# Performance work log

Hardware: AMD Instinct MI355X
Metric: run time of the kernel (lower is better)

The kernel has to match this reference:

```python
import jax, jax.numpy as jnp
import numpy as np

N_NODES = 50000
N_EDGES = 800000


def _gcn_conv(x, W, b, src, dst, deg_inv_sqrt, n_nodes):
    # PyG GCNConv: h = x @ W, then symmetric-normalized sum aggregation
    h = x @ W  # [N, F_out]
    norm = deg_inv_sqrt[src] * deg_inv_sqrt[dst]  # [E_aug]
    msg = h[src] * norm[:, None]  # [E_aug, F_out]
    out = jax.ops.segment_sum(msg, dst, num_segments=n_nodes)
    return out + b


def setup_inputs() -> dict:
    key = jax.random.key(0)
    k1, k2, k3, k4 = jax.random.split(key, 4)
    x = jax.random.normal(k1, (N_NODES, 128), dtype=jnp.float32)
    edge_index = jax.random.randint(k2, (2, N_EDGES), 0, N_NODES, dtype=jnp.int64)
    W1 = jax.random.normal(k3, (128, 64), dtype=jnp.float32) * (1.0 / np.sqrt(128))
    b1 = jnp.zeros((64,), dtype=jnp.float32)
    W2 = jax.random.normal(k4, (64, 32), dtype=jnp.float32) * (1.0 / np.sqrt(64))
    b2 = jnp.zeros((32,), dtype=jnp.float32)
    return {"x": x, "edge_index": edge_index, "W1": W1, "b1": b1, "W2": W2, "b2": b2}


def reference(x, edge_index, W1, b1, W2, b2):
    n_nodes = x.shape[0]
    # add self-loops (PyG GCNConv default)
    loop = jnp.arange(n_nodes, dtype=edge_index.dtype)
    src = jnp.concatenate([edge_index[0], loop])
    dst = jnp.concatenate([edge_index[1], loop])
    # symmetric normalization: deg from target index (gcn_norm)
    deg = jax.ops.segment_sum(jnp.ones_like(dst, dtype=x.dtype), dst, num_segments=n_nodes)
    deg_inv_sqrt = jnp.where(deg > 0, jax.lax.rsqrt(jnp.maximum(deg, 1.0)), 0.0)

    h = _gcn_conv(x, W1, b1, src, dst, deg_inv_sqrt, n_nodes)
    h = jax.nn.relu(h)
    # dropout is identity in eval mode (reference runs inference)
    out = _gcn_conv(h, W2, b2, src, dst, deg_inv_sqrt, n_nodes)
    return out
```

## Files before the change

### kernel.cpp

```cpp
#include <hip/hip_runtime.h>
#include <hip/hip_fp16.h>


#define F_IN 128
#define F_MID 64
#define F_OUT 32
#define NBLK 256

#define RFL(x) __builtin_amdgcn_readfirstlane(x)

__device__ __forceinline__ void h8acc(float* a, const uint4& v) {
    const __half2* hp = (const __half2*)&v;
#pragma unroll
    for (int i = 0; i < 4; ++i) {
        float2 f = __half22float2(hp[i]);
        a[2 * i]     += f.x;
        a[2 * i + 1] += f.y;
    }
}

__device__ __forceinline__ uint4 pack8(const float4& a, const float4& b) {
    union { uint4 u; __half2 h[4]; } pk;
    pk.h[0] = __float22half2_rn(make_float2(a.x, a.y));
    pk.h[1] = __float22half2_rn(make_float2(a.z, a.w));
    pk.h[2] = __float22half2_rn(make_float2(b.x, b.y));
    pk.h[3] = __float22half2_rn(make_float2(b.z, b.w));
    return pk.u;
}

__global__ __launch_bounds__(256) void k_hist(
    const int* __restrict__ dst, int E, int chunk, int nbuk,
    int* __restrict__ blockHist) {
    __shared__ int cnt[256];
    int t = threadIdx.x;
    cnt[t] = 0;
    __syncthreads();
    int e0 = blockIdx.x * chunk;
    int e1 = min(E, e0 + chunk);
    for (int e = e0 + t; e < e1; e += 256)
        atomicAdd(&cnt[dst[e] >> 8], 1);
    __syncthreads();
    if (t < nbuk) blockHist[blockIdx.x * nbuk + t] = cnt[t];
}

__global__ __launch_bounds__(NBLK) void k_scan_buckets(
    const int* __restrict__ blockHist, int nbuk,
    int* __restrict__ blockOff, int* __restrict__ bucketTotal) {
    __shared__ int s[NBLK];
    int b = blockIdx.x;
    int t = threadIdx.x;
    int v = blockHist[t * nbuk + b];
    s[t] = v;
    __syncthreads();
    for (int o = 1; o < NBLK; o <<= 1) {
        int add = (t >= o) ? s[t - o] : 0;
        __syncthreads();
        s[t] += add;
        __syncthreads();
    }
    blockOff[t * nbuk + b] = s[t] - v;
    if (t == NBLK - 1) bucketTotal[b] = s[t];
}

__global__ __launch_bounds__(256) void k_scan_starts(
    const int* __restrict__ bucketTotal, int nbuk, int E,
    int* __restrict__ bucketStart) {
    __shared__ int s[256];
    int t = threadIdx.x;
    int v = (t < nbuk) ? bucketTotal[t] : 0;
    s[t] = v;
    __syncthreads();
    for (int o = 1; o < 256; o <<= 1) {
        int add = (t >= o) ? s[t - o] : 0;
        __syncthreads();
        s[t] += add;
        __syncthreads();
    }
    if (t < nbuk) bucketStart[t] = s[t] - v;
    if (t == 0) bucketStart[nbuk] = E;
}

__global__ __launch_bounds__(256) void k_scatter_edges(
    const int* __restrict__ src, const int* __restrict__ dst, int E, int chunk,
    int nbuk, const int* __restrict__ blockOff, const int* __restrict__ bucketStart,
    int* __restrict__ esort) {
    __shared__ int off[256];
    int t = threadIdx.x;
    if (t < nbuk) off[t] = blockOff[blockIdx.x * nbuk + t] + bucketStart[t];
    __syncthreads();
    int e0 = blockIdx.x * chunk;
    int e1 = min(E, e0 + chunk);
    for (int e = e0 + t; e < e1; e += 256) {
        int d = dst[e];
        int pos = atomicAdd(&off[d >> 8], 1);
        esort[pos] = (src[e] << 8) | (d & 255);
    }
}

__global__ __launch_bounds__(256) void k_bucket_csr(
    const int* __restrict__ esort, const int* __restrict__ bucketStart, int n,
    int* __restrict__ rowstart, int* __restrict__ deg, float* __restrict__ dis,
    int* __restrict__ col) {
    __shared__ int cnt[256];
    __shared__ int s[256];
    __shared__ int cur[256];
    int b = blockIdx.x;
    int t = threadIdx.x;
    int node0 = b << 8;
    int e0 = bucketStart[b], e1 = bucketStart[b + 1];
    cnt[t] = 0;
    __syncthreads();
    for (int e = e0 + t; e < e1; e += 256)
        atomicAdd(&cnt[esort[e] & 255], 1);
    __syncthreads();
    int v = cnt[t];
    s[t] = v;
    __syncthreads();
    for (int o = 1; o < 256; o <<= 1) {
        int add = (t >= o) ? s[t - o] : 0;
        __syncthreads();
        s[t] += add;
        __syncthreads();
    }
    int ex = s[t] - v;
    cur[t] = ex;
    int node = node0 + t;
    if (node < n) {
        rowstart[node] = e0 + ex;
        deg[node] = v;
        dis[node] = rsqrtf((float)(v + 1));
    }
    __syncthreads();
    for (int e = e0 + t; e < e1; e += 256) {
        int p = esort[e];
        int pos = atomicAdd(&cur[p & 255], 1);
        col[e0 + pos] = p >> 8;
    }
}

__global__ __launch_bounds__(256, 4) void k_gemm1(
    const float* __restrict__ x, const float* __restrict__ W1,
    const float* __restrict__ dis, uint4* __restrict__ g1h, int n) {
    __shared__ float xs[64 * 129];
    int tid  = threadIdx.x;
    int row0 = blockIdx.x * 64;
    for (int i = tid; i < 64 * F_IN; i += 256) {
        int r = i >> 7, k = i & 127;
        int gr = row0 + r;
        xs[r * 129 + k] = (gr < n) ? x[(size_t)gr * F_IN + k] : 0.0f;
    }
    __syncthreads();
    int w = RFL(tid >> 6);
    int r = tid & 63;
    const float4* W4 = (const float4*)W1;
    float4 a0 = {0.f,0.f,0.f,0.f}, a1 = a0, a2 = a0, a3 = a0;
#pragma unroll 4
    for (int k = 0; k < F_IN; ++k) {
        float xv = xs[r * 129 + k];
        float4 w0 = W4[k * 16 + w * 4 + 0];
        float4 w1 = W4[k * 16 + w * 4 + 1];
        float4 w2 = W4[k * 16 + w * 4 + 2];
        float4 w3 = W4[k * 16 + w * 4 + 3];
        a0.x += xv * w0.x; a0.y += xv * w0.y; a0.z += xv * w0.z; a0.w += xv * w0.w;
        a1.x += xv * w1.x; a1.y += xv * w1.y; a1.z += xv * w1.z; a1.w += xv * w1.w;
        a2.x += xv * w2.x; a2.y += xv * w2.y; a2.z += xv * w2.z; a2.w += xv * w2.w;
        a3.x += xv * w3.x; a3.y += xv * w3.y; a3.z += xv * w3.z; a3.w += xv * w3.w;
    }
    int gr = row0 + r;
    if (gr < n) {
        float dv = dis[gr];
        a0.x *= dv; a0.y *= dv; a0.z *= dv; a0.w *= dv;
        a1.x *= dv; a1.y *= dv; a1.z *= dv; a1.w *= dv;
        a2.x *= dv; a2.y *= dv; a2.z *= dv; a2.w *= dv;
        a3.x *= dv; a3.y *= dv; a3.z *= dv; a3.w *= dv;
        g1h[(size_t)gr * 8 + w * 2 + 0] = pack8(a0, a1);
        g1h[(size_t)gr * 8 + w * 2 + 1] = pack8(a2, a3);
    }
}

__global__ __launch_bounds__(256) void k_gather1(
    const int* __restrict__ rowstart, const int* __restrict__ deg,
    const int* __restrict__ col, const uint4* __restrict__ g1h,
    const float* __restrict__ dis, const float* __restrict__ b1,
    float* __restrict__ h, int n) {
    int wave = RFL(threadIdx.x >> 6);
    int lane = threadIdx.x & 63;
    int q    = lane & 7;
    int slot = lane >> 3;
    int d    = blockIdx.x * 4 + wave;
    if (d >= n) return;
    int base = RFL(rowstart[d]);
    int cnt  = RFL(deg[d]);
    float a[8] = {0,0,0,0,0,0,0,0};
    float b[8] = {0,0,0,0,0,0,0,0};
    if (slot == 0) {
        uint4 v = g1h[(size_t)d * 8 + q];
        h8acc(a, v);
    }
    int j = 0;
    for (; j + 16 <= cnt; j += 16) {
        int s0 = col[base + j + slot];
        int s1 = col[base + j + 8 + slot];
        uint4 v0 = g1h[(size_t)s0 * 8 + q];
        uint4 v1 = g1h[(size_t)s1 * 8 + q];
        h8acc(a, v0);
        h8acc(b, v1);
    }
    for (; j + 8 <= cnt; j += 8) {
        int s = col[base + j + slot];
        uint4 v = g1h[(size_t)s * 8 + q];
        h8acc(a, v);
    }
    if (slot < cnt - j) {
        int s = col[base + j + slot];
        uint4 v = g1h[(size_t)s * 8 + q];
        h8acc(a, v);
    }
#pragma unroll
    for (int i = 0; i < 8; ++i) a[i] += b[i];
#pragma unroll
    for (int i = 0; i < 8; ++i) a[i] += __shfl_xor(a[i], 8);
#pragma unroll
    for (int i = 0; i < 8; ++i) a[i] += __shfl_xor(a[i], 16);
#pragma unroll
    for (int i = 0; i < 8; ++i) a[i] += __shfl_xor(a[i], 32);
    if (slot == 0) {
        float dv = dis[d];
        float4 bv0 = ((const float4*)b1)[q * 2 + 0];
        float4 bv1 = ((const float4*)b1)[q * 2 + 1];
        float4 o0, o1;
        o0.x = fmaxf(a[0] * dv + bv0.x, 0.f);
        o0.y = fmaxf(a[1] * dv + bv0.y, 0.f);
        o0.z = fmaxf(a[2] * dv + bv0.z, 0.f);
        o0.w = fmaxf(a[3] * dv + bv0.w, 0.f);
        o1.x = fmaxf(a[4] * dv + bv1.x, 0.f);
        o1.y = fmaxf(a[5] * dv + bv1.y, 0.f);
        o1.z = fmaxf(a[6] * dv + bv1.z, 0.f);
        o1.w = fmaxf(a[7] * dv + bv1.w, 0.f);
        float4* H4 = (float4*)h;
        H4[(size_t)d * 16 + q * 2 + 0] = o0;
        H4[(size_t)d * 16 + q * 2 + 1] = o1;
    }
}

__global__ __launch_bounds__(256, 4) void k_gemm2(
    const float* __restrict__ h, const float* __restrict__ W2,
    const float* __restrict__ dis, uint4* __restrict__ g2h, int n) {
    __shared__ float hs[64 * 65];
    int tid  = threadIdx.x;
    int row0 = blockIdx.x * 64;
    for (int i = tid; i < 64 * F_MID; i += 256) {
        int r = i >> 6, k = i & 63;
        int gr = row0 + r;
        hs[r * 65 + k] = (gr < n) ? h[(size_t)gr * F_MID + k] : 0.0f;
    }
    __syncthreads();
    int w = RFL(tid >> 6);
    int r = tid & 63;
    const float4* W4 = (const float4*)W2;
    float4 a0 = {0.f,0.f,0.f,0.f}, a1 = a0;
#pragma unroll 4
    for (int k = 0; k < F_MID; ++k) {
        float hv = hs[r * 65 + k];
        float4 w0 = W4[k * 8 + w * 2 + 0];
        float4 w1 = W4[k * 8 + w * 2 + 1];
        a0.x += hv * w0.x; a0.y += hv * w0.y; a0.z += hv * w0.z; a0.w += hv * w0.w;
        a1.x += hv * w1.x; a1.y += hv * w1.y; a1.z += hv * w1.z; a1.w += hv * w1.w;
    }
    int gr = row0 + r;
    if (gr < n) {
        float dv = dis[gr];
        a0.x *= dv; a0.y *= dv; a0.z *= dv; a0.w *= dv;
        a1.x *= dv; a1.y *= dv; a1.z *= dv; a1.w *= dv;
        g2h[(size_t)gr * 4 + w] = pack8(a0, a1);
    }
}

__global__ __launch_bounds__(256) void k_gather2(
    const int* __restrict__ rowstart, const int* __restrict__ deg,
    const int* __restrict__ col, const uint4* __restrict__ g2h,
    const float* __restrict__ dis, const float* __restrict__ b2,
    float* __restrict__ out, int n) {
    int wave = RFL(threadIdx.x >> 6);
    int lane = threadIdx.x & 63;
    int q    = lane & 3;
    int slot = lane >> 2;
    int d    = blockIdx.x * 4 + wave;
    if (d >= n) return;
    int base = RFL(rowstart[d]);
    int cnt  = RFL(deg[d]);
    float a[8] = {0,0,0,0,0,0,0,0};
    float b[8] = {0,0,0,0,0,0,0,0};
    if (slot == 0) {
        uint4 v = g2h[(size_t)d * 4 + q];
        h8acc(a, v);
    }
    int j = 0;
    for (; j + 32 <= cnt; j += 32) {
        int s0 = col[base + j + slot];
        int s1 = col[base + j + 16 + slot];
        uint4 v0 = g2h[(size_t)s0 * 4 + q];
        uint4 v1 = g2h[(size_t)s1 * 4 + q];
        h8acc(a, v0);
        h8acc(b, v1);
    }
    for (; j + 16 <= cnt; j += 16) {
        int s = col[base + j + slot];
        uint4 v = g2h[(size_t)s * 4 + q];
        h8acc(a, v);
    }
    if (slot < cnt - j) {
        int s = col[base + j + slot];
        uint4 v = g2h[(size_t)s * 4 + q];
        h8acc(a, v);
    }
#pragma unroll
    for (int i = 0; i < 8; ++i) a[i] += b[i];
#pragma unroll
    for (int i = 0; i < 8; ++i) a[i] += __shfl_xor(a[i], 4);
#pragma unroll
    for (int i = 0; i < 8; ++i) a[i] += __shfl_xor(a[i], 8);
#pragma unroll
    for (int i = 0; i < 8; ++i) a[i] += __shfl_xor(a[i], 16);
#pragma unroll
    for (int i = 0; i < 8; ++i) a[i] += __shfl_xor(a[i], 32);
    if (slot == 0) {
        float dv = dis[d];
        float4 bv0 = ((const float4*)b2)[q * 2 + 0];
        float4 bv1 = ((const float4*)b2)[q * 2 + 1];
        float4 o0, o1;
        o0.x = a[0] * dv + bv0.x;
        o0.y = a[1] * dv + bv0.y;
        o0.z = a[2] * dv + bv0.z;
        o0.w = a[3] * dv + bv0.w;
        o1.x = a[4] * dv + bv1.x;
        o1.y = a[5] * dv + bv1.y;
        o1.z = a[6] * dv + bv1.z;
        o1.w = a[7] * dv + bv1.w;
        float4* O4 = (float4*)out;
        O4[(size_t)d * 8 + q * 2 + 0] = o0;
        O4[(size_t)d * 8 + q * 2 + 1] = o1;
    }
}

extern "C" void kernel_launch(void* const* d_in, const int* in_sizes, int n_in,
                              void* d_out, int out_size, void* d_ws, size_t ws_size,
                              hipStream_t stream) {
    const float* x  = (const float*)d_in[0];
    const int*   ei = (const int*)d_in[1];
    const float* W1 = (const float*)d_in[2];
    const float* b1 = (const float*)d_in[3];
    const float* W2 = (const float*)d_in[4];
    const float* b2 = (const float*)d_in[5];

    int n = in_sizes[0] / F_IN;
    int E = in_sizes[1] / 2;
    const int* src = ei;
    const int* dst = ei + E;

    int nbuk  = (n + 255) >> 8;
    int chunk = (E + NBLK - 1) / NBLK;

    char* ws = (char*)d_ws;
    size_t off = 0;
    auto alloc = [&](size_t bytes) {
        char* p = ws + off;
        off += (bytes + 255) & ~(size_t)255;
        return p;
    };
    int*   blockHist   = (int*)  alloc((size_t)NBLK * nbuk * 4);
    int*   blockOff    = (int*)  alloc((size_t)NBLK * nbuk * 4);
    int*   bucketTotal = (int*)  alloc((size_t)nbuk * 4);
    int*   bucketStart = (int*)  alloc((size_t)(nbuk + 1) * 4);
    int*   esort       = (int*)  alloc((size_t)E * 4);
    int*   col         = (int*)  alloc((size_t)E * 4);
    int*   rowstart    = (int*)  alloc((size_t)n * 4);
    int*   deg         = (int*)  alloc((size_t)n * 4);
    float* dis         = (float*)alloc((size_t)n * 4);
    uint4* g1h         = (uint4*)alloc((size_t)n * F_MID * 2);
    float* h           = (float*)alloc((size_t)n * F_MID * 4);
    uint4* g2h         = (uint4*)alloc((size_t)n * F_OUT * 2);

    k_hist<<<NBLK, 256, 0, stream>>>(dst, E, chunk, nbuk, blockHist);
    k_scan_buckets<<<nbuk, NBLK, 0, stream>>>(blockHist, nbuk, blockOff, bucketTotal);
    k_scan_starts<<<1, 256, 0, stream>>>(bucketTotal, nbuk, E, bucketStart);
    k_scatter_edges<<<NBLK, 256, 0, stream>>>(src, dst, E, chunk, nbuk, blockOff,
                                              bucketStart, esort);
    k_bucket_csr<<<nbuk, 256, 0, stream>>>(esort, bucketStart, n, rowstart, deg, dis, col);

    k_gemm1<<<(n + 63) / 64, 256, 0, stream>>>(x, W1, dis, g1h, n);
    k_gather1<<<(n + 3) / 4, 256, 0, stream>>>(rowstart, deg, col, g1h, dis, b1, h, n);
    k_gemm2<<<(n + 63) / 64, 256, 0, stream>>>(h, W2, dis, g2h, n);
    k_gather2<<<(n + 3) / 4, 256, 0, stream>>>(rowstart, deg, col, g2h, dis, b2,
                                               (float*)d_out, n);
}
```

Measured before the change: 184.7 us.

## Replace per-node CSR gather with bucket-level LDS atomic scatter aggregation

Drops the second sorting pass that built a full CSR (rowstart, deg, col) and keeps only the coarse 256-node bucket sort. Each block now owns one bucket of 256 destination nodes, seeds a shared-memory accumulator with the self-loop features, and scatters neighbor features into it with LDS float atomics before applying norm, bias and ReLU. This removes the CSR construction kernel's scan and col writes and the per-node load imbalance. In exchange it adds heavy LDS atomic traffic, a large shared-memory footprint that limits occupancy (about 66KB for layer 1), and only 196 blocks per gather, so there may be too little parallelism to hide latency. Floating-point summation order also becomes nondeterministic.

```diff
diff --git a/kernel.cpp b/kernel.cpp
--- a/kernel.cpp
+++ b/kernel.cpp
@@ -9,13 +9,13 @@
 
 #define RFL(x) __builtin_amdgcn_readfirstlane(x)
 
-__device__ __forceinline__ void h8acc(float* a, const uint4& v) {
+__device__ __forceinline__ void h8unpack(float* f, const uint4& v) {
     const __half2* hp = (const __half2*)&v;
 #pragma unroll
     for (int i = 0; i < 4; ++i) {
-        float2 f = __half22float2(hp[i]);
-        a[2 * i]     += f.x;
-        a[2 * i + 1] += f.y;
+        float2 t = __half22float2(hp[i]);
+        f[2 * i]     = t.x;
+        f[2 * i + 1] = t.y;
     }
 }
 
@@ -97,45 +97,20 @@
     }
 }
 
-__global__ __launch_bounds__(256) void k_bucket_csr(
+__global__ __launch_bounds__(256) void k_deg_dis(
     const int* __restrict__ esort, const int* __restrict__ bucketStart, int n,
-    int* __restrict__ rowstart, int* __restrict__ deg, float* __restrict__ dis,
-    int* __restrict__ col) {
+    float* __restrict__ dis) {
     __shared__ int cnt[256];
-    __shared__ int s[256];
-    __shared__ int cur[256];
     int b = blockIdx.x;
     int t = threadIdx.x;
-    int node0 = b << 8;
+    cnt[t] = 0;
+    __syncthreads();
     int e0 = bucketStart[b], e1 = bucketStart[b + 1];
-    cnt[t] = 0;
-    __syncthreads();
     for (int e = e0 + t; e < e1; e += 256)
         atomicAdd(&cnt[esort[e] & 255], 1);
     __syncthreads();
-    int v = cnt[t];
-    s[t] = v;
-    __syncthreads();
-    for (int o = 1; o < 256; o <<= 1) {
-        int add = (t >= o) ? s[t - o] : 0;
-        __syncthreads();
-        s[t] += add;
-        __syncthreads();
-    }
-    int ex = s[t] - v;
-    cur[t] = ex;
-    int node = node0 + t;
-    if (node < n) {
-        rowstart[node] = e0 + ex;
-        deg[node] = v;
-        dis[node] = rsqrtf((float)(v + 1));
-    }
-    __syncthreads();
-    for (int e = e0 + t; e < e1; e += 256) {
-        int p = esort[e];
-        int pos = atomicAdd(&cur[p & 255], 1);
-        col[e0 + pos] = p >> 8;
-    }
+    int node = (b << 8) + t;
+    if (node < n) dis[node] = rsqrtf((float)(cnt[t] + 1));
 }
 
 __global__ __launch_bounds__(256, 4) void k_gemm1(
@@ -178,68 +153,82 @@
     }
 }
 
-__global__ __launch_bounds__(256) void k_gather1(
-    const int* __restrict__ rowstart, const int* __restrict__ deg,
-    const int* __restrict__ col, const uint4* __restrict__ g1h,
-    const float* __restrict__ dis, const float* __restrict__ b1,
-    float* __restrict__ h, int n) {
-    int wave = RFL(threadIdx.x >> 6);
-    int lane = threadIdx.x & 63;
-    int q    = lane & 7;
-    int slot = lane >> 3;
-    int d    = blockIdx.x * 4 + wave;
-    if (d >= n) return;
-    int base = RFL(rowstart[d]);
-    int cnt  = RFL(deg[d]);
-    float a[8] = {0,0,0,0,0,0,0,0};
-    float b[8] = {0,0,0,0,0,0,0,0};
-    if (slot == 0) {
-        uint4 v = g1h[(size_t)d * 8 + q];
-        h8acc(a, v);
-    }
-    int j = 0;
-    for (; j + 16 <= cnt; j += 16) {
-        int s0 = col[base + j + slot];
-        int s1 = col[base + j + 8 + slot];
-        uint4 v0 = g1h[(size_t)s0 * 8 + q];
-        uint4 v1 = g1h[(size_t)s1 * 8 + q];
-        h8acc(a, v0);
-        h8acc(b, v1);
-    }
-    for (; j + 8 <= cnt; j += 8) {
-        int s = col[base + j + slot];
-        uint4 v = g1h[(size_t)s * 8 + q];
-        h8acc(a, v);
-    }
-    if (slot < cnt - j) {
-        int s = col[base + j + slot];
-        uint4 v = g1h[(size_t)s * 8 + q];
-        h8acc(a, v);
-    }
-#pragma unroll
-    for (int i = 0; i < 8; ++i) a[i] += b[i];
-#pragma unroll
-    for (int i = 0; i < 8; ++i) a[i] += __shfl_xor(a[i], 8);
-#pragma unroll
-    for (int i = 0; i < 8; ++i) a[i] += __shfl_xor(a[i], 16);
-#pragma unroll
-    for (int i = 0; i < 8; ++i) a[i] += __shfl_xor(a[i], 32);
-    if (slot == 0) {
-        float dv = dis[d];
-        float4 bv0 = ((const float4*)b1)[q * 2 + 0];
-        float4 bv1 = ((const float4*)b1)[q * 2 + 1];
-        float4 o0, o1;
-        o0.x = fmaxf(a[0] * dv + bv0.x, 0.f);
-        o0.y = fmaxf(a[1] * dv + bv0.y, 0.f);
-        o0.z = fmaxf(a[2] * dv + bv0.z, 0.f);
-        o0.w = fmaxf(a[3] * dv + bv0.w, 0.f);
-        o1.x = fmaxf(a[4] * dv + bv1.x, 0.f);
-        o1.y = fmaxf(a[5] * dv + bv1.y, 0.f);
-        o1.z = fmaxf(a[6] * dv + bv1.z, 0.f);
-        o1.w = fmaxf(a[7] * dv + bv1.w, 0.f);
-        float4* H4 = (float4*)h;
-        H4[(size_t)d * 16 + q * 2 + 0] = o0;
-        H4[(size_t)d * 16 + q * 2 + 1] = o1;
+__global__ __launch_bounds__(256) void k_bgather1(
+    const int* __restrict__ esort, const int* __restrict__ bucketStart,
+    const uint4* __restrict__ g1h, const float* __restrict__ dis,
+    const float* __restrict__ b1, float4* __restrict__ h4, int n) {
+    __shared__ float acc[256 * 65];
+    int b = blockIdx.x;
+    int t = threadIdx.x;
+    int node0 = b << 8;
+    for (int i = t; i < 256 * 8; i += 256) {
+        int dloc = i >> 3, q = i & 7;
+        int node = node0 + dloc;
+        float f[8] = {0,0,0,0,0,0,0,0};
+        if (node < n) {
+            uint4 v = g1h[(size_t)node * 8 + q];
+            h8unpack(f, v);
+        }
+        float* base = &acc[dloc * 65 + q * 8];
+#pragma unroll
+        for (int k = 0; k < 8; ++k) base[k] = f[k];
+    }
+    __syncthreads();
+    int e0 = bucketStart[b], e1 = bucketStart[b + 1];
+    int wave = RFL(t >> 6);
+    int lane = t & 63;
+    int slot = lane & 7;
+    int q    = lane >> 3;
+    int e = e0 + wave * 16;
+    for (; e + 16 <= e1; e += 64) {
+        int pA = esort[e + slot];
+        int pB = esort[e + 8 + slot];
+        uint4 vA = g1h[(size_t)(pA >> 8) * 8 + q];
+        uint4 vB = g1h[(size_t)(pB >> 8) * 8 + q];
+        float fA[8], fB[8];
+        h8unpack(fA, vA);
+        h8unpack(fB, vB);
+        float* bA = &acc[(pA & 255) * 65 + q * 8];
+        float* bB = &acc[(pB & 255) * 65 + q * 8];
+#pragma unroll
+        for (int k = 0; k < 8; ++k) atomicAdd(&bA[k], fA[k]);
+#pragma unroll
+        for (int k = 0; k < 8; ++k) atomicAdd(&bB[k], fB[k]);
+    }
+    int rem = e1 - e;
+    if (slot < rem) {
+        int p = esort[e + slot];
+        uint4 v = g1h[(size_t)(p >> 8) * 8 + q];
+        float f[8];
+        h8unpack(f, v);
+        float* ba = &acc[(p & 255) * 65 + q * 8];
+#pragma unroll
+        for (int k = 0; k < 8; ++k) atomicAdd(&ba[k], f[k]);
+    }
+    if (8 + slot < rem) {
+        int p = esort[e + 8 + slot];
+        uint4 v = g1h[(size_t)(p >> 8) * 8 + q];
+        float f[8];
+        h8unpack(f, v);
+        float* ba = &acc[(p & 255) * 65 + q * 8];
+#pragma unroll
+        for (int k = 0; k < 8; ++k) atomicAdd(&ba[k], f[k]);
+    }
+    __syncthreads();
+    const float4* B4 = (const float4*)b1;
+    for (int i = t; i < 256 * 16; i += 256) {
+        int dloc = i >> 4, c = i & 15;
+        int node = node0 + dloc;
+        if (node >= n) continue;
+        float dv = dis[node];
+        float* ap = &acc[dloc * 65 + c * 4];
+        float4 bv = B4[c];
+        float4 o;
+        o.x = fmaxf(ap[0] * dv + bv.x, 0.f);
+        o.y = fmaxf(ap[1] * dv + bv.y, 0.f);
+        o.z = fmaxf(ap[2] * dv + bv.z, 0.f);
+        o.w = fmaxf(ap[3] * dv + bv.w, 0.f);
+        h4[(size_t)node * 16 + c] = o;
     }
 }
 
@@ -276,70 +265,82 @@
     }
 }
 
-__global__ __launch_bounds__(256) void k_gather2(
-    const int* __restrict__ rowstart, const int* __restrict__ deg,
-    const int* __restrict__ col, const uint4* __restrict__ g2h,
-    const float* __restrict__ dis, const float* __restrict__ b2,
-    float* __restrict__ out, int n) {
-    int wave = RFL(threadIdx.x >> 6);
-    int lane = threadIdx.x & 63;
-    int q    = lane & 3;
-    int slot = lane >> 2;
-    int d    = blockIdx.x * 4 + wave;
-    if (d >= n) return;
-    int base = RFL(rowstart[d]);
-    int cnt  = RFL(deg[d]);
-    float a[8] = {0,0,0,0,0,0,0,0};
-    float b[8] = {0,0,0,0,0,0,0,0};
-    if (slot == 0) {
-        uint4 v = g2h[(size_t)d * 4 + q];
-        h8acc(a, v);
-    }
-    int j = 0;
-    for (; j + 32 <= cnt; j += 32) {
-        int s0 = col[base + j + slot];
-        int s1 = col[base + j + 16 + slot];
-        uint4 v0 = g2h[(size_t)s0 * 4 + q];
-        uint4 v1 = g2h[(size_t)s1 * 4 + q];
-        h8acc(a, v0);
-        h8acc(b, v1);
-    }
-    for (; j + 16 <= cnt; j += 16) {
-        int s = col[base + j + slot];
-        uint4 v = g2h[(size_t)s * 4 + q];
-        h8acc(a, v);
-    }
-    if (slot < cnt - j) {
-        int s = col[base + j + slot];
-        uint4 v = g2h[(size_t)s * 4 + q];
-        h8acc(a, v);
-    }
-#pragma unroll
-    for (int i = 0; i < 8; ++i) a[i] += b[i];
-#pragma unroll
-    for (int i = 0; i < 8; ++i) a[i] += __shfl_xor(a[i], 4);
-#pragma unroll
-    for (int i = 0; i < 8; ++i) a[i] += __shfl_xor(a[i], 8);
-#pragma unroll
-    for (int i = 0; i < 8; ++i) a[i] += __shfl_xor(a[i], 16);
-#pragma unroll
-    for (int i = 0; i < 8; ++i) a[i] += __shfl_xor(a[i], 32);
-    if (slot == 0) {
-        float dv = dis[d];
-        float4 bv0 = ((const float4*)b2)[q * 2 + 0];
-        float4 bv1 = ((const float4*)b2)[q * 2 + 1];
-        float4 o0, o1;
-        o0.x = a[0] * dv + bv0.x;
-        o0.y = a[1] * dv + bv0.y;
-        o0.z = a[2] * dv + bv0.z;
-        o0.w = a[3] * dv + bv0.w;
-        o1.x = a[4] * dv + bv1.x;
-        o1.y = a[5] * dv + bv1.y;
-        o1.z = a[6] * dv + bv1.z;
-        o1.w = a[7] * dv + bv1.w;
-        float4* O4 = (float4*)out;
-        O4[(size_t)d * 8 + q * 2 + 0] = o0;
-        O4[(size_t)d * 8 + q * 2 + 1] = o1;
+__global__ __launch_bounds__(256) void k_bgather2(
+    const int* __restrict__ esort, const int* __restrict__ bucketStart,
+    const uint4* __restrict__ g2h, const float* __restrict__ dis,
+    const float* __restrict__ b2, float4* __restrict__ out4, int n) {
+    __shared__ float acc[256 * 33];
+    int b = blockIdx.x;
+    int t = threadIdx.x;
+    int node0 = b << 8;
+    for (int i = t; i < 256 * 4; i += 256) {
+        int dloc = i >> 2, q = i & 3;
+        int node = node0 + dloc;
+        float f[8] = {0,0,0,0,0,0,0,0};
+        if (node < n) {
+            uint4 v = g2h[(size_t)node * 4 + q];
+            h8unpack(f, v);
+        }
+        float* base = &acc[dloc * 33 + q * 8];
+#pragma unroll
+        for (int k = 0; k < 8; ++k) base[k] = f[k];
+    }
+    __syncthreads();
+    int e0 = bucketStart[b], e1 = bucketStart[b + 1];
+    int wave = RFL(t >> 6);
+    int lane = t & 63;
+    int slot = lane & 15;
+    int q    = lane >> 4;
+    int e = e0 + wave * 32;
+    for (; e + 32 <= e1; e += 128) {
+        int pA = esort[e + slot];
+        int pB = esort[e + 16 + slot];
+        uint4 vA = g2h[(size_t)(pA >> 8) * 4 + q];
+        uint4 vB = g2h[(size_t)(pB >> 8) * 4 + q];
+        float fA[8], fB[8];
+        h8unpack(fA, vA);
+        h8unpack(fB, vB);
+        float* bA = &acc[(pA & 255) * 33 + q * 8];
+        float* bB = &acc[(pB & 255) * 33 + q * 8];
+#pragma unroll
+        for (int k = 0; k < 8; ++k) atomicAdd(&bA[k], fA[k]);
+#pragma unroll
+        for (int k = 0; k < 8; ++k) atomicAdd(&bB[k], fB[k]);
+    }
+    int rem = e1 - e;
+    if (slot < rem) {
+        int p = esort[e + slot];
+        uint4 v = g2h[(size_t)(p >> 8) * 4 + q];
+        float f[8];
+        h8unpack(f, v);
+        float* ba = &acc[(p & 255) * 33 + q * 8];
+#pragma unroll
+        for (int k = 0; k < 8; ++k) atomicAdd(&ba[k], f[k]);
+    }
+    if (16 + slot < rem) {
+        int p = esort[e + 16 + slot];
+        uint4 v = g2h[(size_t)(p >> 8) * 4 + q];
+        float f[8];
+        h8unpack(f, v);
+        float* ba = &acc[(p & 255) * 33 + q * 8];
+#pragma unroll
+        for (int k = 0; k < 8; ++k) atomicAdd(&ba[k], f[k]);
+    }
+    __syncthreads();
+    const float4* B4 = (const float4*)b2;
+    for (int i = t; i < 256 * 8; i += 256) {
+        int dloc = i >> 3, c = i & 7;
+        int node = node0 + dloc;
+        if (node >= n) continue;
+        float dv = dis[node];
+        float* ap = &acc[dloc * 33 + c * 4];
+        float4 bv = B4[c];
+        float4 o;
+        o.x = ap[0] * dv + bv.x;
+        o.y = ap[1] * dv + bv.y;
+        o.z = ap[2] * dv + bv.z;
+        o.w = ap[3] * dv + bv.w;
+        out4[(size_t)node * 8 + c] = o;
     }
 }
 
@@ -373,9 +374,6 @@
     int*   bucketTotal = (int*)  alloc((size_t)nbuk * 4);
     int*   bucketStart = (int*)  alloc((size_t)(nbuk + 1) * 4);
     int*   esort       = (int*)  alloc((size_t)E * 4);
-    int*   col         = (int*)  alloc((size_t)E * 4);
-    int*   rowstart    = (int*)  alloc((size_t)n * 4);
-    int*   deg         = (int*)  alloc((size_t)n * 4);
     float* dis         = (float*)alloc((size_t)n * 4);
     uint4* g1h         = (uint4*)alloc((size_t)n * F_MID * 2);
     float* h           = (float*)alloc((size_t)n * F_MID * 4);
@@ -386,11 +384,12 @@
     k_scan_starts<<<1, 256, 0, stream>>>(bucketTotal, nbuk, E, bucketStart);
     k_scatter_edges<<<NBLK, 256, 0, stream>>>(src, dst, E, chunk, nbuk, blockOff,
                                               bucketStart, esort);
-    k_bucket_csr<<<nbuk, 256, 0, stream>>>(esort, bucketStart, n, rowstart, deg, dis, col);
+    k_deg_dis<<<nbuk, 256, 0, stream>>>(esort, bucketStart, n, dis);
 
     k_gemm1<<<(n + 63) / 64, 256, 0, stream>>>(x, W1, dis, g1h, n);
-    k_gather1<<<(n + 3) / 4, 256, 0, stream>>>(rowstart, deg, col, g1h, dis, b1, h, n);
+    k_bgather1<<<nbuk, 256, 0, stream>>>(esort, bucketStart, g1h, dis, b1,
+                                         (float4*)h, n);
     k_gemm2<<<(n + 63) / 64, 256, 0, stream>>>(h, W2, dis, g2h, n);
-    k_gather2<<<(n + 3) / 4, 256, 0, stream>>>(rowstart, deg, col, g2h, dis, b2,
-                                               (float*)d_out, n);
-}
+    k_bgather2<<<nbuk, 256, 0, stream>>>(esort, bucketStart, g2h, dis, b2,
+                                         (float4*)d_out, n);
+}
```

After: 669.2 us. 262% more time.
